# Kernel tuning notes

Measured on AMD Instinct MI355X. Metric: run time of the kernel, lower is better.

## Reference

```python
import jax, jax.numpy as jnp
import numpy as np

N_HEAD = 16
MASK_NEG = 1e10  # matches torch's -10000000000.0 * (1 - b)


def setup_inputs() -> dict:
    key = jax.random.key(0)
    ks = jax.random.split(key, 9)
    B, S, D = 2, 2048, 2048
    std = 0.02
    inp = {
        "x": jax.random.normal(ks[0], (B, S, D), dtype=jnp.float32),
        "Wq": jax.random.normal(ks[1], (D, D), dtype=jnp.float32) * std,
        "bq": jnp.zeros((D,), dtype=jnp.float32),
        "Wk": jax.random.normal(ks[2], (D, D), dtype=jnp.float32) * std,
        "bk": jnp.zeros((D,), dtype=jnp.float32),
        "Wv": jax.random.normal(ks[3], (D, D), dtype=jnp.float32) * std,
        "bv": jnp.zeros((D,), dtype=jnp.float32),
        "Wd": jax.random.normal(ks[4], (D, D), dtype=jnp.float32) * std,
        "bd": jnp.zeros((D,), dtype=jnp.float32),
    }
    return inp


def reference(x, Wq, bq, Wk, bk, Wv, bv, Wd, bd):
    # x: [B, S, D]; layer_past=None, query=None path (full causal prefill)
    B, S, D = x.shape
    H = N_HEAD
    hd = D // H

    def split(h):  # [B,S,D] -> [B,H,S,hd]
        return h.reshape(B, S, H, hd).transpose(0, 2, 1, 3)

    q = split(x @ Wq + bq)
    k = split(x @ Wk + bk)
    v = split(x @ Wv + bv)

    # scores [B,H,S,S]; scale=True divides by sqrt(head_dim)
    w = jnp.einsum("bhqd,bhkd->bhqk", q, k) / jnp.sqrt(jnp.float32(hd))
    b = jnp.tril(jnp.ones((S, S), dtype=w.dtype))  # causal bias buffer slice
    w = w * b - MASK_NEG * (1.0 - b)
    w = jax.nn.softmax(w, axis=-1)
    a = jnp.einsum("bhqk,bhkd->bhqd", w, v)

    a = a.transpose(0, 2, 1, 3).reshape(B, S, D)  # merge_heads
    a = a @ Wd + bd
    present = jnp.stack((k, v))  # [2, B, H, S, hd]
    return a, present
```

## Files before the change

### kernel.cpp

```cpp
#include <hip/hip_runtime.h>


typedef unsigned short ushort_t;
typedef __attribute__((ext_vector_type(8))) short short8;
typedef __attribute__((ext_vector_type(4))) float f32x4;

#define MFMA16x16x32 __builtin_amdgcn_mfma_f32_16x16x32_bf16
#define S_LEN   2048
#define DMODEL  2048
#define A_ELEMS 8388608
#define W_ELEMS 4194304

__device__ __forceinline__ ushort_t f2bf(float x) {
  unsigned u = __float_as_uint(x);
  u += 0x7FFFu + ((u >> 16) & 1u);
  return (ushort_t)(u >> 16);
}
__device__ __forceinline__ unsigned pack2(float lo, float hi) {
  return (unsigned)f2bf(lo) | ((unsigned)f2bf(hi) << 16);
}
struct f8 { float v[8]; };
__device__ __forceinline__ f8 ld8f(const float* p) {
  f8 r;
  float4 a = *(const float4*)p, b = *(const float4*)(p + 4);
  r.v[0]=a.x; r.v[1]=a.y; r.v[2]=a.z; r.v[3]=a.w;
  r.v[4]=b.x; r.v[5]=b.y; r.v[6]=b.z; r.v[7]=b.w;
  return r;
}
__device__ __forceinline__ uint4 cvt8(const f8& f) {
  uint4 o;
  o.x = pack2(f.v[0], f.v[1]); o.y = pack2(f.v[2], f.v[3]);
  o.z = pack2(f.v[4], f.v[5]); o.w = pack2(f.v[6], f.v[7]);
  return o;
}

typedef const __attribute__((address_space(1))) void* gas_t;
typedef __attribute__((address_space(3))) void* las_t;
__device__ __forceinline__ void gld16(const void* g, void* l) {
  __builtin_amdgcn_global_load_lds((gas_t)(unsigned long long)g,
                                   (las_t)(unsigned)(unsigned long long)l,
                                   16, 0, 0);
}

__global__ void __launch_bounds__(256) conv_x(const float* __restrict__ x,
                                              ushort_t* __restrict__ xb) {
  const int i = (blockIdx.x * 256 + threadIdx.x) * 8;
  f8 v = ld8f(x + i);
  *(uint4*)&xb[i] = cvt8(v);
}

__global__ void __launch_bounds__(256) trans_w(
    const float* __restrict__ w0, const float* __restrict__ w1,
    const float* __restrict__ w2, const float* __restrict__ w3,
    ushort_t* __restrict__ o0, ushort_t* __restrict__ o1,
    ushort_t* __restrict__ o2, ushort_t* __restrict__ o3) {
  __shared__ float t[64][65];
  const float* src; ushort_t* dst;
  switch (blockIdx.z) {
    case 0: src = w0; dst = o0; break;
    case 1: src = w1; dst = o1; break;
    case 2: src = w2; dst = o2; break;
    default: src = w3; dst = o3; break;
  }
  const int kb = blockIdx.y * 64, nb = blockIdx.x * 64;
  const int r = threadIdx.x >> 3, c8 = (threadIdx.x & 7) * 8;
#pragma unroll
  for (int i = 0; i < 64; i += 32) {
    *(float4*)&t[r + i][c8]     = *(const float4*)&src[(size_t)(kb + r + i) * DMODEL + nb + c8];
    *(float4*)&t[r + i][c8 + 4] = *(const float4*)&src[(size_t)(kb + r + i) * DMODEL + nb + c8 + 4];
  }
  __syncthreads();
#pragma unroll
  for (int i = 0; i < 64; i += 32) {
    float tmp[8];
#pragma unroll
    for (int j = 0; j < 8; ++j) tmp[j] = t[c8 + j][r + i];
    uint4 o;
    o.x = pack2(tmp[0], tmp[1]); o.y = pack2(tmp[2], tmp[3]);
    o.z = pack2(tmp[4], tmp[5]); o.w = pack2(tmp[6], tmp[7]);
    *(uint4*)&dst[(size_t)(nb + r + i) * DMODEL + kb + c8] = o;
  }
}

__global__ void __launch_bounds__(256) trans_v(const float* __restrict__ v,
                                               ushort_t* __restrict__ vt) {
  __shared__ float t[64][65];
  const int bh = blockIdx.z;
  const int sb = blockIdx.x * 64, db = blockIdx.y * 64;
  const float* src = v + (size_t)bh * S_LEN * 128;
  ushort_t* dst = vt + (size_t)bh * 128 * S_LEN;
  const int r = threadIdx.x >> 3, c8 = (threadIdx.x & 7) * 8;
#pragma unroll
  for (int i = 0; i < 64; i += 32) {
    *(float4*)&t[r + i][c8]     = *(const float4*)&src[(size_t)(sb + r + i) * 128 + db + c8];
    *(float4*)&t[r + i][c8 + 4] = *(const float4*)&src[(size_t)(sb + r + i) * 128 + db + c8 + 4];
  }
  __syncthreads();
#pragma unroll
  for (int i = 0; i < 64; i += 32) {
    float tmp[8];
#pragma unroll
    for (int j = 0; j < 8; ++j) tmp[j] = t[c8 + j][r + i];
    uint4 o;
    o.x = pack2(tmp[0], tmp[1]); o.y = pack2(tmp[2], tmp[3]);
    o.z = pack2(tmp[4], tmp[5]); o.w = pack2(tmp[6], tmp[7]);
    *(uint4*)&dst[(size_t)(db + r + i) * S_LEN + sb + c8] = o;
  }
}

__device__ __forceinline__ void gemm_core(
    const ushort_t* __restrict__ gA, const ushort_t* __restrict__ gB,
    ushort_t* As, ushort_t* Bs, int w, int lane, int wr, int wc,
    f32x4 acc[4][4]) {
  const int sr = lane >> 2, sc = (lane & 3) * 8;
  const int l15 = lane & 15, quad = lane >> 4;
  const ushort_t* pA = gA + sc;
  const ushort_t* pB = gB + sc;
  for (int kt = 0; kt < 2048; kt += 32) {
    __syncthreads();
#pragma unroll
    for (int i = 0; i < 4; ++i) {
      const int c = i * 4 + w;
      if (c < 8)
        gld16(pA + (size_t)(c * 16 + sr) * 2048 + kt, (void*)(As + c * 512));
      else
        gld16(pB + (size_t)((c - 8) * 16 + sr) * 2048 + kt,
              (void*)(Bs + (c - 8) * 512));
    }
    __syncthreads();
    short8 af[4], bf[4];
#pragma unroll
    for (int mi = 0; mi < 4; ++mi)
      af[mi] = *(const short8*)&As[(wr + mi * 16 + l15) * 32 + quad * 8];
#pragma unroll
    for (int ni = 0; ni < 4; ++ni)
      bf[ni] = *(const short8*)&Bs[(wc + ni * 16 + l15) * 32 + quad * 8];
#pragma unroll
    for (int mi = 0; mi < 4; ++mi)
#pragma unroll
      for (int ni = 0; ni < 4; ++ni)
        acc[mi][ni] = MFMA16x16x32(af[mi], bf[ni], acc[mi][ni], 0, 0, 0);
  }
}

__global__ void __launch_bounds__(256) gemm_qkv(
    const ushort_t* __restrict__ xb,
    const ushort_t* __restrict__ wtq, const ushort_t* __restrict__ wtk,
    const ushort_t* __restrict__ wtv,
    const float* __restrict__ bq, const float* __restrict__ bk,
    const float* __restrict__ bv,
    ushort_t* __restrict__ qout, float* __restrict__ kout,
    float* __restrict__ vout, ushort_t* __restrict__ kb16) {
  __shared__ ushort_t As[4096], Bs[4096];
  const int tid = threadIdx.x, w = tid >> 6, lane = tid & 63;
  const int l15 = lane & 15, quad = lane >> 4;
  const int bx = blockIdx.x, wid = bx >> 9, r = bx & 511;
  const int tm = r & 31, tn = r >> 5;
  const int wr = (w >> 1) * 64, wc = (w & 1) * 64;
  const ushort_t* Wt = wid == 0 ? wtq : (wid == 1 ? wtk : wtv);
  const float* bias = wid == 0 ? bq : (wid == 1 ? bk : bv);

  f32x4 acc[4][4] = {};
  gemm_core(xb + (size_t)(tm * 128) * 2048, Wt + (size_t)(tn * 128) * 2048,
            As, Bs, w, lane, wr, wc, acc);

  const int row0 = tm * 128 + wr, col0 = tn * 128 + wc;
#pragma unroll
  for (int ni = 0; ni < 4; ++ni) {
    const int col = col0 + ni * 16 + l15;
    const float bv_ = bias[col];
    const int h = col >> 7, d = col & 127;
#pragma unroll
    for (int mi = 0; mi < 4; ++mi) {
#pragma unroll
      for (int j = 0; j < 4; ++j) {
        const int row = row0 + mi * 16 + quad * 4 + j;
        const int b = row >> 11, s = row & 2047;
        const size_t idx = (size_t)(((b * 16 + h) * 2048 + s)) * 128 + d;
        const float v = acc[mi][ni][j] + bv_;
        if (wid == 0) qout[idx] = f2bf(v);
        else if (wid == 1) { kout[idx] = v; kb16[idx] = f2bf(v); }
        else vout[idx] = v;
      }
    }
  }
}

__global__ void __launch_bounds__(256) gemm_proj(
    const ushort_t* __restrict__ A, const ushort_t* __restrict__ Wt,
    const float* __restrict__ bias, float* __restrict__ C) {
  __shared__ ushort_t As[4096], Bs[4096];
  const int tid = threadIdx.x, w = tid >> 6, lane = tid & 63;
  const int l15 = lane & 15, quad = lane >> 4;
  const int tm = blockIdx.x & 31, tn = blockIdx.x >> 5;
  const int wr = (w >> 1) * 64, wc = (w & 1) * 64;

  f32x4 acc[4][4] = {};
  gemm_core(A + (size_t)(tm * 128) * 2048, Wt + (size_t)(tn * 128) * 2048,
            As, Bs, w, lane, wr, wc, acc);

  const int row0 = tm * 128 + wr, col0 = tn * 128 + wc;
#pragma unroll
  for (int ni = 0; ni < 4; ++ni) {
    const int col = col0 + ni * 16 + l15;
    const float bv_ = bias[col];
#pragma unroll
    for (int mi = 0; mi < 4; ++mi)
#pragma unroll
      for (int j = 0; j < 4; ++j) {
        const int row = row0 + mi * 16 + quad * 4 + j;
        C[(size_t)row * DMODEL + col] = acc[mi][ni][j] + bv_;
      }
  }
}

__global__ void __launch_bounds__(512, 2) attn_fwd(
    const ushort_t* __restrict__ Q, const ushort_t* __restrict__ Kb,
    const ushort_t* __restrict__ Vt, ushort_t* __restrict__ O) {
  __shared__ ushort_t KP[128 * 136];
  __shared__ ushort_t Vs[128 * 128];
  const int tid = threadIdx.x;
  const int w = tid >> 6, lane = tid & 63;
  const int l15 = lane & 15, quad = lane >> 4;
  const int x7 = l15 & 7;
  const int bh = blockIdx.x & 31, pr = blockIdx.x >> 5;
  const int b = bh >> 4, h = bh & 15;
  const size_t base  = (size_t)bh * (S_LEN * 128);
  const size_t vbase = (size_t)bh * (128 * S_LEN);
  const float cs = 0.08838834764831845f * 1.4426950408889634f;

  const int srow = lane >> 4;
  const int schunk = lane & 15;

  for (int seg = 0; seg < 2; ++seg) {
    const int qt = (seg == 0) ? (15 - pr) : pr;
    const int q0 = qt * 128 + w * 16;

    short8 qf[4];
#pragma unroll
    for (int ks = 0; ks < 4; ++ks)
      qf[ks] = *(const short8*)&Q[base + (size_t)(q0 + l15) * 128 + ks * 32 + quad * 8];

    f32x4 oacc[8] = {};
    float mrun[4], lrun[4];
#pragma unroll
    for (int j = 0; j < 4; ++j) { mrun[j] = -1e30f; lrun[j] = 0.f; }

    for (int kt = 0; kt <= qt; ++kt) {
      const int kb_ = kt * 128;
      __syncthreads();
#pragma unroll
      for (int i = 0; i < 4; ++i) {
        const int r = w * 16 + i * 4 + srow;
        const int c = schunk ^ (r & 7);
        gld16(Kb + base + (size_t)(kb_ + r) * 128 + c * 8,
              (void*)(KP + (w * 16 + i * 4) * 128));
        gld16(Vt + vbase + (size_t)r * S_LEN + kb_ + c * 8,
              (void*)(Vs + (w * 16 + i * 4) * 128));
      }
      __syncthreads();

      f32x4 sacc[8] = {};
#pragma unroll
      for (int ks = 0; ks < 4; ++ks) {
        const int sw = ((ks * 4 + quad) ^ x7) * 8;
        short8 kf[8];
#pragma unroll
        for (int ni = 0; ni < 8; ++ni)
          kf[ni] = *(const short8*)&KP[(ni * 16 + l15) * 128 + sw];
#pragma unroll
        for (int ni = 0; ni < 8; ++ni)
          sacc[ni] = MFMA16x16x32(qf[ks], kf[ni], sacc[ni], 0, 0, 0);
      }
      __syncthreads();

#pragma unroll
      for (int j = 0; j < 4; ++j) {
        const int rl = quad * 4 + j;
        const int rowg = q0 + rl;
        float t0[8];
#pragma unroll
        for (int ni = 0; ni < 8; ++ni) {
          const int kg = kb_ + ni * 16 + l15;
          const float s = sacc[ni][j] * cs;
          t0[ni] = (kg <= rowg) ? s : -1e30f;
        }
        float rm = fmaxf(fmaxf(fmaxf(t0[0], t0[1]), fmaxf(t0[2], t0[3])),
                         fmaxf(fmaxf(t0[4], t0[5]), fmaxf(t0[6], t0[7])));
        rm = fmaxf(rm, __shfl_xor(rm, 1));
        rm = fmaxf(rm, __shfl_xor(rm, 2));
        rm = fmaxf(rm, __shfl_xor(rm, 4));
        rm = fmaxf(rm, __shfl_xor(rm, 8));
        const float mold = mrun[j];
        const float mnew = fmaxf(mold, rm);
        const float alpha = __builtin_amdgcn_exp2f(mold - mnew);
        float rs = 0.f;
#pragma unroll
        for (int ni = 0; ni < 8; ++ni) {
          const float pe = __builtin_amdgcn_exp2f(t0[ni] - mnew);
          rs += pe;
          KP[(w * 16 + rl) * 136 + ni * 16 + l15] = f2bf(pe);
        }
        rs += __shfl_xor(rs, 1);
        rs += __shfl_xor(rs, 2);
        rs += __shfl_xor(rs, 4);
        rs += __shfl_xor(rs, 8);
        lrun[j] = lrun[j] * alpha + rs;
        mrun[j] = mnew;
#pragma unroll
        for (int oi = 0; oi < 8; ++oi) oacc[oi][j] *= alpha;
      }

#pragma unroll
      for (int ks = 0; ks < 4; ++ks) {
        const int sw = ((ks * 4 + quad) ^ x7) * 8;
        short8 pf = *(const short8*)&KP[(w * 16 + l15) * 136 + ks * 32 + quad * 8];
        short8 vf[8];
#pragma unroll
        for (int oi = 0; oi < 8; ++oi)
          vf[oi] = *(const short8*)&Vs[(oi * 16 + l15) * 128 + sw];
#pragma unroll
        for (int oi = 0; oi < 8; ++oi)
          oacc[oi] = MFMA16x16x32(pf, vf[oi], oacc[oi], 0, 0, 0);
      }
    }

    {
      float inv[4];
#pragma unroll
      for (int j = 0; j < 4; ++j) inv[j] = 1.f / lrun[j];
#pragma unroll
      for (int oi = 0; oi < 8; ++oi) {
        const int oc = oi * 16 + l15;
#pragma unroll
        for (int j = 0; j < 4; ++j) {
          const int s = q0 + quad * 4 + j;
          O[((size_t)(b * S_LEN + s)) * DMODEL + h * 128 + oc] =
              f2bf(oacc[oi][j] * inv[j]);
        }
      }
    }
  }
}

extern "C" void kernel_launch(void* const* d_in, const int* in_sizes, int n_in,
                              void* d_out, int out_size, void* d_ws,
                              size_t ws_size, hipStream_t stream) {
  const float* x  = (const float*)d_in[0];
  const float* Wq = (const float*)d_in[1];
  const float* bq = (const float*)d_in[2];
  const float* Wk = (const float*)d_in[3];
  const float* bk = (const float*)d_in[4];
  const float* Wv = (const float*)d_in[5];
  const float* bv = (const float*)d_in[6];
  const float* Wd = (const float*)d_in[7];
  const float* bd = (const float*)d_in[8];

  float* out   = (float*)d_out;
  float* a_out = out;
  float* k_out = out + A_ELEMS;
  float* v_out = out + 2 * A_ELEMS;
  ushort_t* ob  = (ushort_t*)d_out;
  ushort_t* xb   = ob;
  ushort_t* q_ws = ob + A_ELEMS;

  ushort_t* ws  = (ushort_t*)d_ws;
  ushort_t* wtq = ws;
  ushort_t* wtk = ws + W_ELEMS;
  ushort_t* wtv = ws + 2 * (size_t)W_ELEMS;
  ushort_t* wtd = ws + 3 * (size_t)W_ELEMS;
  ushort_t* attn_ws = ws + 4 * (size_t)W_ELEMS;
  ushort_t* kb_ws   = attn_ws + (size_t)A_ELEMS;
  ushort_t* vt_ws   = attn_ws + 2 * (size_t)A_ELEMS;

  conv_x<<<4096, 256, 0, stream>>>(x, xb);
  trans_w<<<dim3(32, 32, 4), 256, 0, stream>>>(Wq, Wk, Wv, Wd,
                                               wtq, wtk, wtv, wtd);
  gemm_qkv<<<1536, 256, 0, stream>>>(xb, wtq, wtk, wtv, bq, bk, bv,
                                     q_ws, k_out, v_out, kb_ws);
  trans_v<<<dim3(32, 2, 32), 256, 0, stream>>>(v_out, vt_ws);
  attn_fwd<<<256, 512, 0, stream>>>(q_ws, kb_ws, vt_ws, attn_ws);
  gemm_proj<<<512, 256, 0, stream>>>(attn_ws, wtd, bd, a_out);
}
```

Baseline: 455.0 us.

## Rewrite GEMM core as double-buffered 256x128 tile with XOR-swizzled LDS

Replaces the single-buffered 128x128, 4-wave GEMM mainloop with a 512-thread, 256x128 tile kernel. It prefetches the next K-slices into a second LDS buffer while MFMAs run, raises MFMA priority with s_setprio, and applies an XOR swizzle to LDS slots to avoid bank conflicts. The intent is to hide global-load latency, cut barrier stalls and raise operand reuse for the QKV and output projections. In exchange it uses more LDS and registers per block, launches half as many blocks, and relies on hand-counted vmcnt waits that must match the issued loads exactly.

```diff
diff --git a/kernel.cpp b/kernel.cpp
--- a/kernel.cpp
+++ b/kernel.cpp
@@ -108,42 +108,82 @@
   }
 }
 
-__device__ __forceinline__ void gemm_core(
+#define BUFA (2 * 256 * 32)
+#define BUFB (2 * 128 * 32)
+
+__device__ __forceinline__ void stage3(
     const ushort_t* __restrict__ gA, const ushort_t* __restrict__ gB,
-    ushort_t* As, ushort_t* Bs, int w, int lane, int wr, int wc,
-    f32x4 acc[4][4]) {
-  const int sr = lane >> 2, sc = (lane & 3) * 8;
+    ushort_t* Ab, ushort_t* Bb, int tile, int ks, int w, size_t a_off) {
+  const size_t kc = (size_t)(tile * 64 + ks * 32);
+  gld16(gA + (size_t)(w * 16) * 2048 + kc + a_off,
+        Ab + (ks * 256 + w * 16) * 32);
+  gld16(gA + (size_t)((w + 8) * 16) * 2048 + kc + a_off,
+        Ab + (ks * 256 + (w + 8) * 16) * 32);
+  gld16(gB + (size_t)(w * 16) * 2048 + kc + a_off,
+        Bb + (ks * 128 + w * 16) * 32);
+}
+
+__device__ __forceinline__ void gemm8p_core(
+    const ushort_t* __restrict__ gA, const ushort_t* __restrict__ gB,
+    ushort_t* AsF, ushort_t* BsF, int w, int lane, f32x4 acc[8][2]) {
   const int l15 = lane & 15, quad = lane >> 4;
-  const ushort_t* pA = gA + sc;
-  const ushort_t* pB = gB + sc;
-  for (int kt = 0; kt < 2048; kt += 32) {
-    __syncthreads();
-#pragma unroll
-    for (int i = 0; i < 4; ++i) {
-      const int c = i * 4 + w;
-      if (c < 8)
-        gld16(pA + (size_t)(c * 16 + sr) * 2048 + kt, (void*)(As + c * 512));
-      else
-        gld16(pB + (size_t)((c - 8) * 16 + sr) * 2048 + kt,
-              (void*)(Bs + (c - 8) * 512));
-    }
-    __syncthreads();
-    short8 af[4], bf[4];
-#pragma unroll
-    for (int mi = 0; mi < 4; ++mi)
-      af[mi] = *(const short8*)&As[(wr + mi * 16 + l15) * 32 + quad * 8];
-#pragma unroll
-    for (int ni = 0; ni < 4; ++ni)
-      bf[ni] = *(const short8*)&Bs[(wc + ni * 16 + l15) * 32 + quad * 8];
-#pragma unroll
-    for (int mi = 0; mi < 4; ++mi)
-#pragma unroll
-      for (int ni = 0; ni < 4; ++ni)
+  const int wm = w >> 2, wn = w & 3;
+  const size_t a_off = (size_t)(lane >> 2) * 2048 +
+                       (((lane & 3) ^ ((lane >> 3) & 3)) * 8);
+  const int rslot8 = (quad ^ ((l15 >> 1) & 3)) * 8;
+  const int arow = wm * 128 + l15;
+  const int brow = wn * 32 + l15;
+
+  stage3(gA, gB, AsF, BsF, 0, 0, w, a_off);
+  stage3(gA, gB, AsF, BsF, 0, 1, w, a_off);
+  stage3(gA, gB, AsF + BUFA, BsF + BUFB, 1, 0, w, a_off);
+  asm volatile("s_waitcnt vmcnt(3)" ::: "memory");
+  asm volatile("s_barrier" ::: "memory");
+
+  for (int t = 0; t < 32; ++t) {
+    ushort_t* Ab  = AsF + (t & 1) * BUFA;
+    ushort_t* Bb  = BsF + (t & 1) * BUFB;
+    ushort_t* Abn = AsF + ((t + 1) & 1) * BUFA;
+    ushort_t* Bbn = BsF + ((t + 1) & 1) * BUFB;
+    short8 af[8], bf[2];
+#pragma unroll
+    for (int mi = 0; mi < 8; ++mi)
+      af[mi] = *(const short8*)&Ab[(arow + mi * 16) * 32 + rslot8];
+#pragma unroll
+    for (int ni = 0; ni < 2; ++ni)
+      bf[ni] = *(const short8*)&Bb[(brow + ni * 16) * 32 + rslot8];
+    if (t + 1 < 32) stage3(gA, gB, Abn, Bbn, t + 1, 1, w, a_off);
+    asm volatile("s_barrier" ::: "memory");
+    __builtin_amdgcn_s_setprio(1);
+#pragma unroll
+    for (int mi = 0; mi < 8; ++mi)
+#pragma unroll
+      for (int ni = 0; ni < 2; ++ni)
         acc[mi][ni] = MFMA16x16x32(af[mi], bf[ni], acc[mi][ni], 0, 0, 0);
-  }
-}
-
-__global__ void __launch_bounds__(256) gemm_qkv(
+    __builtin_amdgcn_s_setprio(0);
+    asm volatile("s_barrier" ::: "memory");
+#pragma unroll
+    for (int mi = 0; mi < 8; ++mi)
+      af[mi] = *(const short8*)&Ab[(256 * 32) + (arow + mi * 16) * 32 + rslot8];
+#pragma unroll
+    for (int ni = 0; ni < 2; ++ni)
+      bf[ni] = *(const short8*)&Bb[(128 * 32) + (brow + ni * 16) * 32 + rslot8];
+    if (t + 2 < 32) stage3(gA, gB, Ab, Bb, t + 2, 0, w, a_off);
+    asm volatile("s_barrier" ::: "memory");
+    __builtin_amdgcn_s_setprio(1);
+#pragma unroll
+    for (int mi = 0; mi < 8; ++mi)
+#pragma unroll
+      for (int ni = 0; ni < 2; ++ni)
+        acc[mi][ni] = MFMA16x16x32(af[mi], bf[ni], acc[mi][ni], 0, 0, 0);
+    __builtin_amdgcn_s_setprio(0);
+    if (t < 30)       asm volatile("s_waitcnt vmcnt(3)" ::: "memory");
+    else if (t == 30) asm volatile("s_waitcnt vmcnt(0)" ::: "memory");
+    asm volatile("s_barrier" ::: "memory");
+  }
+}
+
+__global__ void __launch_bounds__(512, 2) gemm_qkv(
     const ushort_t* __restrict__ xb,
     const ushort_t* __restrict__ wtq, const ushort_t* __restrict__ wtk,
     const ushort_t* __restrict__ wtv,
@@ -151,61 +191,63 @@
     const float* __restrict__ bv,
     ushort_t* __restrict__ qout, float* __restrict__ kout,
     float* __restrict__ vout, ushort_t* __restrict__ kb16) {
-  __shared__ ushort_t As[4096], Bs[4096];
+  __shared__ ushort_t As_[2 * BUFA];
+  __shared__ ushort_t Bs_[2 * BUFB];
   const int tid = threadIdx.x, w = tid >> 6, lane = tid & 63;
   const int l15 = lane & 15, quad = lane >> 4;
-  const int bx = blockIdx.x, wid = bx >> 9, r = bx & 511;
-  const int tm = r & 31, tn = r >> 5;
-  const int wr = (w >> 1) * 64, wc = (w & 1) * 64;
+  const int wm = w >> 2, wn = w & 3;
+  const int bx = blockIdx.x, wid = bx >> 8, idx = bx & 255;
+  const int tm = idx & 15, tn = idx >> 4;
   const ushort_t* Wt = wid == 0 ? wtq : (wid == 1 ? wtk : wtv);
   const float* bias = wid == 0 ? bq : (wid == 1 ? bk : bv);
 
-  f32x4 acc[4][4] = {};
-  gemm_core(xb + (size_t)(tm * 128) * 2048, Wt + (size_t)(tn * 128) * 2048,
-            As, Bs, w, lane, wr, wc, acc);
-
-  const int row0 = tm * 128 + wr, col0 = tn * 128 + wc;
-#pragma unroll
-  for (int ni = 0; ni < 4; ++ni) {
+  f32x4 acc[8][2] = {};
+  gemm8p_core(xb + (size_t)(tm * 256) * 2048, Wt + (size_t)(tn * 128) * 2048,
+              As_, Bs_, w, lane, acc);
+
+  const int row0 = tm * 256 + wm * 128, col0 = tn * 128 + wn * 32;
+#pragma unroll
+  for (int ni = 0; ni < 2; ++ni) {
     const int col = col0 + ni * 16 + l15;
     const float bv_ = bias[col];
     const int h = col >> 7, d = col & 127;
 #pragma unroll
-    for (int mi = 0; mi < 4; ++mi) {
+    for (int mi = 0; mi < 8; ++mi) {
 #pragma unroll
       for (int j = 0; j < 4; ++j) {
         const int row = row0 + mi * 16 + quad * 4 + j;
         const int b = row >> 11, s = row & 2047;
-        const size_t idx = (size_t)(((b * 16 + h) * 2048 + s)) * 128 + d;
+        const size_t idxg = (size_t)(((b * 16 + h) * 2048 + s)) * 128 + d;
         const float v = acc[mi][ni][j] + bv_;
-        if (wid == 0) qout[idx] = f2bf(v);
-        else if (wid == 1) { kout[idx] = v; kb16[idx] = f2bf(v); }
-        else vout[idx] = v;
+        if (wid == 0) qout[idxg] = f2bf(v);
+        else if (wid == 1) { kout[idxg] = v; kb16[idxg] = f2bf(v); }
+        else vout[idxg] = v;
       }
     }
   }
 }
 
-__global__ void __launch_bounds__(256) gemm_proj(
+__global__ void __launch_bounds__(512, 2) gemm_proj(
     const ushort_t* __restrict__ A, const ushort_t* __restrict__ Wt,
     const float* __restrict__ bias, float* __restrict__ C) {
-  __shared__ ushort_t As[4096], Bs[4096];
+  __shared__ ushort_t As_[2 * BUFA];
+  __shared__ ushort_t Bs_[2 * BUFB];
   const int tid = threadIdx.x, w = tid >> 6, lane = tid & 63;
   const int l15 = lane & 15, quad = lane >> 4;
-  const int tm = blockIdx.x & 31, tn = blockIdx.x >> 5;
-  const int wr = (w >> 1) * 64, wc = (w & 1) * 64;
-
-  f32x4 acc[4][4] = {};
-  gemm_core(A + (size_t)(tm * 128) * 2048, Wt + (size_t)(tn * 128) * 2048,
-            As, Bs, w, lane, wr, wc, acc);
-
-  const int row0 = tm * 128 + wr, col0 = tn * 128 + wc;
-#pragma unroll
-  for (int ni = 0; ni < 4; ++ni) {
+  const int wm = w >> 2, wn = w & 3;
+  const int tm = blockIdx.x & 15, tn = blockIdx.x >> 4;
+
+  f32x4 acc[8][2] = {};
+  gemm8p_core(A + (size_t)(tm * 256) * 2048, Wt + (size_t)(tn * 128) * 2048,
+              As_, Bs_, w, lane, acc);
+
+  const int row0 = tm * 256 + wm * 128, col0 = tn * 128 + wn * 32;
+#pragma unroll
+  for (int ni = 0; ni < 2; ++ni) {
     const int col = col0 + ni * 16 + l15;
     const float bv_ = bias[col];
 #pragma unroll
-    for (int mi = 0; mi < 4; ++mi)
+    for (int mi = 0; mi < 8; ++mi)
 #pragma unroll
       for (int j = 0; j < 4; ++j) {
         const int row = row0 + mi * 16 + quad * 4 + j;
@@ -376,9 +418,9 @@
   conv_x<<<4096, 256, 0, stream>>>(x, xb);
   trans_w<<<dim3(32, 32, 4), 256, 0, stream>>>(Wq, Wk, Wv, Wd,
                                                wtq, wtk, wtv, wtd);
-  gemm_qkv<<<1536, 256, 0, stream>>>(xb, wtq, wtk, wtv, bq, bk, bv,
-                                     q_ws, k_out, v_out, kb_ws);
+  gemm_qkv<<<768, 512, 0, stream>>>(xb, wtq, wtk, wtv, bq, bk, bv,
+                                    q_ws, k_out, v_out, kb_ws);
   trans_v<<<dim3(32, 2, 32), 256, 0, stream>>>(v_out, vt_ws);
   attn_fwd<<<256, 512, 0, stream>>>(q_ws, kb_ws, vt_ws, attn_ws);
-  gemm_proj<<<512, 256, 0, stream>>>(attn_ws, wtd, bd, a_out);
-}
+  gemm_proj<<<256, 512, 0, stream>>>(attn_ws, wtd, bd, a_out);
+}
```

Measured after the change: 445.2 us. 1.02x faster.

## Rework GEMM core with double-buffered 128x256 tiles, swizzled LDS, and XCD-aware block mapping

Applied to the files above, without the earlier changes.

Both projection GEMMs switch from a single-buffered 128x128 tile with BK=32 and two barriers per step to a 512-thread, 128x256 tile with BK=64. Global-to-LDS loads are double buffered so the next K-slice streams in while MFMAs run on the current one. LDS columns are XOR-swizzled to cut bank conflicts. Block indices are remapped so neighbouring tiles land on the same XCD, and s_setprio raises wave priority around the MFMA bursts. The cost is more LDS per block (96 KB), fewer blocks, and more registers per wave, which may reduce occupancy.

```diff
diff --git a/kernel.cpp b/kernel.cpp
--- a/kernel.cpp
+++ b/kernel.cpp
@@ -108,42 +108,69 @@
   }
 }
 
-__device__ __forceinline__ void gemm_core(
+#define ABUF (2 * 128 * 32)
+#define BBUF (2 * 256 * 32)
+
+__device__ __forceinline__ void stage6(
     const ushort_t* __restrict__ gA, const ushort_t* __restrict__ gB,
-    ushort_t* As, ushort_t* Bs, int w, int lane, int wr, int wc,
-    f32x4 acc[4][4]) {
-  const int sr = lane >> 2, sc = (lane & 3) * 8;
+    ushort_t* An, ushort_t* Bn, int t, int w, size_t soff) {
+  const size_t kc = (size_t)t * 64;
+#pragma unroll
+  for (int i = 0; i < 2; ++i) {
+    const int c = 2 * w + i, kh = c >> 3, rg = c & 7;
+    gld16(gA + (size_t)(rg * 16) * 2048 + kc + kh * 32 + soff,
+          An + (kh * 128 + rg * 16) * 32);
+  }
+#pragma unroll
+  for (int i = 0; i < 4; ++i) {
+    const int c = 4 * w + i, kh = c >> 4, rg = c & 15;
+    gld16(gB + (size_t)(rg * 16) * 2048 + kc + kh * 32 + soff,
+          Bn + (kh * 256 + rg * 16) * 32);
+  }
+}
+
+__device__ __forceinline__ void gemm2p_core(
+    const ushort_t* __restrict__ gA, const ushort_t* __restrict__ gB,
+    ushort_t* AsF, ushort_t* BsF, int w, int lane, f32x4 acc[4][4]) {
   const int l15 = lane & 15, quad = lane >> 4;
-  const ushort_t* pA = gA + sc;
-  const ushort_t* pB = gB + sc;
-  for (int kt = 0; kt < 2048; kt += 32) {
-    __syncthreads();
-#pragma unroll
-    for (int i = 0; i < 4; ++i) {
-      const int c = i * 4 + w;
-      if (c < 8)
-        gld16(pA + (size_t)(c * 16 + sr) * 2048 + kt, (void*)(As + c * 512));
-      else
-        gld16(pB + (size_t)((c - 8) * 16 + sr) * 2048 + kt,
-              (void*)(Bs + (c - 8) * 512));
+  const int wm = w >> 2, wn = w & 3;
+  const size_t soff = (size_t)(lane >> 2) * 2048 +
+                      (((lane & 3) ^ ((lane >> 3) & 3)) * 8);
+  const int rslot8 = (quad ^ ((l15 >> 1) & 3)) * 8;
+  const int arow = wm * 64 + l15;
+  const int brow = wn * 64 + l15;
+
+  stage6(gA, gB, AsF, BsF, 0, w, soff);
+  __syncthreads();
+
+  for (int t = 0; t < 32; ++t) {
+    ushort_t* Ab = AsF + (t & 1) * ABUF;
+    ushort_t* Bb = BsF + (t & 1) * BBUF;
+    if (t + 1 < 32)
+      stage6(gA, gB, AsF + ((t + 1) & 1) * ABUF, BsF + ((t + 1) & 1) * BBUF,
+             t + 1, w, soff);
+#pragma unroll
+    for (int kh = 0; kh < 2; ++kh) {
+      short8 af[4], bf[4];
+#pragma unroll
+      for (int mi = 0; mi < 4; ++mi)
+        af[mi] = *(const short8*)&Ab[(kh * 128 + arow + mi * 16) * 32 + rslot8];
+#pragma unroll
+      for (int ni = 0; ni < 4; ++ni)
+        bf[ni] = *(const short8*)&Bb[(kh * 256 + brow + ni * 16) * 32 + rslot8];
+      __builtin_amdgcn_s_setprio(1);
+#pragma unroll
+      for (int mi = 0; mi < 4; ++mi)
+#pragma unroll
+        for (int ni = 0; ni < 4; ++ni)
+          acc[mi][ni] = MFMA16x16x32(af[mi], bf[ni], acc[mi][ni], 0, 0, 0);
+      __builtin_amdgcn_s_setprio(0);
     }
     __syncthreads();
-    short8 af[4], bf[4];
-#pragma unroll
-    for (int mi = 0; mi < 4; ++mi)
-      af[mi] = *(const short8*)&As[(wr + mi * 16 + l15) * 32 + quad * 8];
-#pragma unroll
-    for (int ni = 0; ni < 4; ++ni)
-      bf[ni] = *(const short8*)&Bs[(wc + ni * 16 + l15) * 32 + quad * 8];
-#pragma unroll
-    for (int mi = 0; mi < 4; ++mi)
-#pragma unroll
-      for (int ni = 0; ni < 4; ++ni)
-        acc[mi][ni] = MFMA16x16x32(af[mi], bf[ni], acc[mi][ni], 0, 0, 0);
-  }
-}
-
-__global__ void __launch_bounds__(256) gemm_qkv(
+  }
+}
+
+__global__ void __launch_bounds__(512, 2) gemm_qkv(
     const ushort_t* __restrict__ xb,
     const ushort_t* __restrict__ wtq, const ushort_t* __restrict__ wtk,
     const ushort_t* __restrict__ wtv,
@@ -151,20 +178,23 @@
     const float* __restrict__ bv,
     ushort_t* __restrict__ qout, float* __restrict__ kout,
     float* __restrict__ vout, ushort_t* __restrict__ kb16) {
-  __shared__ ushort_t As[4096], Bs[4096];
+  __shared__ ushort_t As_[2 * ABUF];
+  __shared__ ushort_t Bs_[2 * BBUF];
   const int tid = threadIdx.x, w = tid >> 6, lane = tid & 63;
   const int l15 = lane & 15, quad = lane >> 4;
-  const int bx = blockIdx.x, wid = bx >> 9, r = bx & 511;
-  const int tm = r & 31, tn = r >> 5;
-  const int wr = (w >> 1) * 64, wc = (w & 1) * 64;
+  const int wm = w >> 2, wn = w & 3;
+  const int bx = blockIdx.x;
+  const int logical = (bx & 7) * 96 + (bx >> 3);
+  const int wid = logical >> 8, idx = logical & 255;
+  const int tn = idx & 7, tm = idx >> 3;
   const ushort_t* Wt = wid == 0 ? wtq : (wid == 1 ? wtk : wtv);
   const float* bias = wid == 0 ? bq : (wid == 1 ? bk : bv);
 
   f32x4 acc[4][4] = {};
-  gemm_core(xb + (size_t)(tm * 128) * 2048, Wt + (size_t)(tn * 128) * 2048,
-            As, Bs, w, lane, wr, wc, acc);
-
-  const int row0 = tm * 128 + wr, col0 = tn * 128 + wc;
+  gemm2p_core(xb + (size_t)(tm * 128) * 2048, Wt + (size_t)(tn * 256) * 2048,
+              As_, Bs_, w, lane, acc);
+
+  const int row0 = tm * 128 + wm * 64, col0 = tn * 256 + wn * 64;
 #pragma unroll
   for (int ni = 0; ni < 4; ++ni) {
     const int col = col0 + ni * 16 + l15;
@@ -176,30 +206,32 @@
       for (int j = 0; j < 4; ++j) {
         const int row = row0 + mi * 16 + quad * 4 + j;
         const int b = row >> 11, s = row & 2047;
-        const size_t idx = (size_t)(((b * 16 + h) * 2048 + s)) * 128 + d;
+        const size_t idxg = (size_t)(((b * 16 + h) * 2048 + s)) * 128 + d;
         const float v = acc[mi][ni][j] + bv_;
-        if (wid == 0) qout[idx] = f2bf(v);
-        else if (wid == 1) { kout[idx] = v; kb16[idx] = f2bf(v); }
-        else vout[idx] = v;
+        if (wid == 0) qout[idxg] = f2bf(v);
+        else if (wid == 1) { kout[idxg] = v; kb16[idxg] = f2bf(v); }
+        else vout[idxg] = v;
       }
     }
   }
 }
 
-__global__ void __launch_bounds__(256) gemm_proj(
+__global__ void __launch_bounds__(512, 2) gemm_proj(
     const ushort_t* __restrict__ A, const ushort_t* __restrict__ Wt,
     const float* __restrict__ bias, float* __restrict__ C) {
-  __shared__ ushort_t As[4096], Bs[4096];
+  __shared__ ushort_t As_[2 * ABUF];
+  __shared__ ushort_t Bs_[2 * BBUF];
   const int tid = threadIdx.x, w = tid >> 6, lane = tid & 63;
   const int l15 = lane & 15, quad = lane >> 4;
-  const int tm = blockIdx.x & 31, tn = blockIdx.x >> 5;
-  const int wr = (w >> 1) * 64, wc = (w & 1) * 64;
+  const int wm = w >> 2, wn = w & 3;
+  const int logical = (blockIdx.x & 7) * 32 + (blockIdx.x >> 3);
+  const int tn = logical & 7, tm = logical >> 3;
 
   f32x4 acc[4][4] = {};
-  gemm_core(A + (size_t)(tm * 128) * 2048, Wt + (size_t)(tn * 128) * 2048,
-            As, Bs, w, lane, wr, wc, acc);
-
-  const int row0 = tm * 128 + wr, col0 = tn * 128 + wc;
+  gemm2p_core(A + (size_t)(tm * 128) * 2048, Wt + (size_t)(tn * 256) * 2048,
+              As_, Bs_, w, lane, acc);
+
+  const int row0 = tm * 128 + wm * 64, col0 = tn * 256 + wn * 64;
 #pragma unroll
   for (int ni = 0; ni < 4; ++ni) {
     const int col = col0 + ni * 16 + l15;
@@ -376,9 +408,9 @@
   conv_x<<<4096, 256, 0, stream>>>(x, xb);
   trans_w<<<dim3(32, 32, 4), 256, 0, stream>>>(Wq, Wk, Wv, Wd,
                                                wtq, wtk, wtv, wtd);
-  gemm_qkv<<<1536, 256, 0, stream>>>(xb, wtq, wtk, wtv, bq, bk, bv,
-                                     q_ws, k_out, v_out, kb_ws);
+  gemm_qkv<<<768, 512, 0, stream>>>(xb, wtq, wtk, wtv, bq, bk, bv,
+                                    q_ws, k_out, v_out, kb_ws);
   trans_v<<<dim3(32, 2, 32), 256, 0, stream>>>(v_out, vt_ws);
   attn_fwd<<<256, 512, 0, stream>>>(q_ws, kb_ws, vt_ws, attn_ws);
-  gemm_proj<<<512, 256, 0, stream>>>(attn_ws, wtd, bd, a_out);
-}
+  gemm_proj<<<256, 512, 0, stream>>>(attn_ws, wtd, bd, a_out);
+}
```

New measurement: 446.6 us. Within noise of the previous version (-1.9%).
